# Optimization experiments

Measured on AMD Instinct MI355X. Metric: run time of the kernel, lower is better.

Reference implementation:

```python
import jax, jax.numpy as jnp
import numpy as np

LAMBDA_ENERGY = 0.1
LAMBDA_COV = 0.005
TWO_PI = 2.0 * np.pi
EPS = 1e-12


def setup_inputs() -> dict:
    key = jax.random.key(0)
    k1, k2, k3, k4 = jax.random.split(key, 4)
    B, T, C, D, K, F = 32, 1024, 8, 8, 8, 64
    x = jax.random.normal(k1, (B, T, C, F), dtype=jnp.float32)
    x_hat = jax.random.normal(k2, (B, T, C, F), dtype=jnp.float32)
    z = jax.random.normal(k3, (B, T, C, D), dtype=jnp.float32)
    # gamma is a mixture-responsibility tensor (softmax output in DAGMM)
    gamma = jax.nn.softmax(jax.random.uniform(k4, (B, T, C, K), dtype=jnp.float32) * 4.0, axis=-1)
    return {"x": x, "x_hat": x_hat, "z": z, "gamma": gamma}


def _gmm_energy(z, gamma):
    # z: [B,T,C,D], gamma: [B,T,C,K]
    N = gamma.shape[0] * gamma.shape[1] * gamma.shape[2]
    gsum = jnp.sum(gamma, axis=(0, 1, 2))                      # [K]
    phi = gsum / N                                             # [K]
    mu = jnp.einsum('btck,btcd->kd', gamma, z) / gsum[:, None]  # [K,D]
    z_mu = z[..., None, :] - mu                                # [B,T,C,K,D]
    cov = jnp.einsum('btck,btcki,btckj->kij', gamma, z_mu, z_mu) / gsum[:, None, None]  # [K,D,D]

    D = cov.shape[-1]
    cov_k = cov + EPS * jnp.eye(D, dtype=cov.dtype)            # [K,D,D]
    cov_inv = jnp.linalg.inv(cov_k)                            # batched small-matrix inverse
    L = jnp.linalg.cholesky(TWO_PI * cov_k)                    # [K,D,D]
    det_cov = jnp.prod(jnp.diagonal(L, axis1=-2, axis2=-1), axis=-1)  # [K], = sqrt(det(2*pi*cov))
    cov_diag = jnp.sum(1.0 / jnp.diagonal(cov_k, axis1=-2, axis2=-1))

    # quadratic form per sample/component: [B,T,C,K]
    quad = jnp.einsum('btcki,kij,btckj->btck', z_mu, cov_inv, z_mu)
    E = jnp.exp(-0.5 * quad)
    E_z = -jnp.log(jnp.sum(phi * E / jnp.sqrt(det_cov), axis=-1) + EPS)
    return jnp.mean(E_z), cov_diag


def reference(x, x_hat, z, gamma):
    reconst_loss = jnp.mean((x_hat - x) ** 2)
    sample_energy, cov_diag = _gmm_energy(z, gamma)
    return reconst_loss + LAMBDA_ENERGY * sample_energy + LAMBDA_COV * cov_diag
```

## Files before the change

kernel.cpp:

```cpp
#include <hip/hip_runtime.h>
#include <math.h>

#define WS_RED   0
#define WS_EN    2048
#define WS_MU    2304
#define WS_CINV  2368
#define WS_COEF  2880
#define WS_CD    2888
#define WS_STATP 4096

static constexpr int NSAMP = 32 * 1024 * 8;
static constexpr int NX4   = NSAMP * 64 / 4;
static constexpr int RE_BLOCKS   = 2048;
static constexpr int STAT_BLOCKS = 256;
static constexpr int EN_BLOCKS   = 256;
static constexpr float EPSF = 1e-12f;

__device__ inline float wave_reduce_sum(float v) {
    #pragma unroll
    for (int m = 1; m < 64; m <<= 1) v += __shfl_xor(v, m, 64);
    return v;
}
__device__ inline double wave_reduce_sum_d(double v) {
    #pragma unroll
    for (int m = 1; m < 64; m <<= 1) v += __shfl_xor(v, m, 64);
    return v;
}

__global__ __launch_bounds__(256) void krecon(const float4* __restrict__ x,
                                              const float4* __restrict__ xh,
                                              float* __restrict__ ws) {
    __shared__ float lds[4];
    float acc = 0.f;
    const int t = blockIdx.x * 256 + threadIdx.x;
    #pragma unroll 4
    for (int i = 0; i < 8; ++i) {
        int idx = t + i * (RE_BLOCKS * 256);
        float4 a = x[idx], b = xh[idx];
        float d0 = b.x - a.x, d1 = b.y - a.y, d2 = b.z - a.z, d3 = b.w - a.w;
        acc = fmaf(d0, d0, acc);
        acc = fmaf(d1, d1, acc);
        acc = fmaf(d2, d2, acc);
        acc = fmaf(d3, d3, acc);
    }
    acc = wave_reduce_sum(acc);
    int w = threadIdx.x >> 6;
    if ((threadIdx.x & 63) == 0) lds[w] = acc;
    __syncthreads();
    if (threadIdx.x == 0)
        ws[WS_RED + blockIdx.x] = lds[0] + lds[1] + lds[2] + lds[3];
}

__global__ __launch_bounds__(256) void kstats(const float4* __restrict__ z4,
                                              const float* __restrict__ gamma,
                                              float* __restrict__ ws) {
    __shared__ float lds[4][360];
    float acc[45];
    #pragma unroll
    for (int i = 0; i < 45; ++i) acc[i] = 0.f;

    const int k    = threadIdx.x & 7;
    const int grp  = (blockIdx.x << 5) | (threadIdx.x >> 3);
    constexpr int NGRP  = STAT_BLOCKS << 5;
    constexpr int ITERS = NSAMP / NGRP;

    for (int it = 0; it < ITERS; ++it) {
        int n = grp + it * NGRP;
        float4 a = z4[n * 2], b = z4[n * 2 + 1];
        float zv[8] = {a.x, a.y, a.z, a.w, b.x, b.y, b.z, b.w};
        float g = gamma[n * 8 + k];
        acc[0] += g;
        float gz[8];
        #pragma unroll
        for (int i = 0; i < 8; ++i) { gz[i] = g * zv[i]; acc[1 + i] += gz[i]; }
        #pragma unroll
        for (int i = 0; i < 8; ++i) {
            #pragma unroll
            for (int j = 0; j < 8; ++j) {
                if (j <= i)
                    acc[9 + (i * (i + 1)) / 2 + j] =
                        fmaf(gz[i], zv[j], acc[9 + (i * (i + 1)) / 2 + j]);
            }
        }
    }

    #pragma unroll
    for (int i = 0; i < 45; ++i) {
        float v = acc[i];
        v += __shfl_xor(v, 8, 64);
        v += __shfl_xor(v, 16, 64);
        v += __shfl_xor(v, 32, 64);
        acc[i] = v;
    }
    int lane = threadIdx.x & 63, w = threadIdx.x >> 6;
    if (lane < 8) {
        #pragma unroll
        for (int i = 0; i < 45; ++i) lds[w][lane * 45 + i] = acc[i];
    }
    __syncthreads();
    for (int v = threadIdx.x; v < 360; v += 256) {
        ws[WS_STATP + blockIdx.x * 360 + v] =
            lds[0][v] + lds[1][v] + lds[2][v] + lds[3][v];
    }
}

__global__ void kfinalize(float* __restrict__ ws) {
    __shared__ double sstat[360];
    for (int v = threadIdx.x; v < 360; v += 512) {
        double s = 0.0;
        for (int b = 0; b < STAT_BLOCKS; ++b)
            s += (double)ws[WS_STATP + b * 360 + v];
        sstat[v] = s;
    }
    __syncthreads();

    int k = threadIdx.x;
    if (k < 8) {
        const double* st = &sstat[k * 45];
        double g = st[0];
        double mu[8];
        for (int d = 0; d < 8; ++d) mu[d] = st[1 + d] / g;
        double A[8][8];
        {
            int t = 0;
            for (int i = 0; i < 8; ++i)
                for (int j = 0; j <= i; ++j) {
                    double v = st[9 + t] / g - mu[i] * mu[j];
                    A[i][j] = v; A[j][i] = v; ++t;
                }
        }
        for (int d = 0; d < 8; ++d) A[d][d] += (double)EPSF;

        double cd = 0.0;
        for (int d = 0; d < 8; ++d) cd += 1.0 / A[d][d];
        ws[WS_CD + k] = (float)cd;

        double L[8][8] = {};
        for (int i = 0; i < 8; ++i) {
            for (int j = 0; j <= i; ++j) {
                double s = A[i][j];
                for (int p = 0; p < j; ++p) s -= L[i][p] * L[j][p];
                if (i == j) L[i][i] = sqrt(s);
                else        L[i][j] = s / L[j][j];
            }
        }
        double M[8][8] = {};
        for (int i = 0; i < 8; ++i) {
            M[i][i] = 1.0 / L[i][i];
            for (int j = 0; j < i; ++j) {
                double s = 0.0;
                for (int p = j; p < i; ++p) s -= L[i][p] * M[p][j];
                M[i][j] = s / L[i][i];
            }
        }
        for (int i = 0; i < 8; ++i)
            for (int j = 0; j < 8; ++j) {
                double s = 0.0;
                int p0 = i > j ? i : j;
                for (int p = p0; p < 8; ++p) s += M[p][i] * M[p][j];
                ws[WS_CINV + k * 64 + i * 8 + j] = (float)s;
            }

        double det = 1.0;
        for (int d = 0; d < 8; ++d) det *= L[d][d];
        double c = 2.0 * M_PI;
        det *= c * c * c * c;
        double phi = g / (double)NSAMP;
        ws[WS_COEF + k] = (float)(phi / sqrt(det));
        for (int d = 0; d < 8; ++d) ws[WS_MU + k * 8 + d] = (float)mu[d];
    }
}

__global__ __launch_bounds__(256, 4) void kenergy(const float4* __restrict__ z4,
                                                  float* __restrict__ ws) {
    __shared__ float smu[64], scinv[512], scoef[8];
    __shared__ float lds[4];
    for (int i = threadIdx.x; i < 64; i += 256) smu[i] = ws[WS_MU + i];
    for (int i = threadIdx.x; i < 512; i += 256) scinv[i] = ws[WS_CINV + i];
    if (threadIdx.x < 8) scoef[threadIdx.x] = ws[WS_COEF + threadIdx.x];
    __syncthreads();

    const int base = blockIdx.x * 1024 + threadIdx.x;
    float zv[4][8];
    #pragma unroll
    for (int s = 0; s < 4; ++s) {
        int n = base + s * 256;
        float4 a = z4[n * 2], b = z4[n * 2 + 1];
        zv[s][0] = a.x; zv[s][1] = a.y; zv[s][2] = a.z; zv[s][3] = a.w;
        zv[s][4] = b.x; zv[s][5] = b.y; zv[s][6] = b.z; zv[s][7] = b.w;
    }
    float sacc[4] = {0.f, 0.f, 0.f, 0.f};

    #pragma unroll 1
    for (int k = 0; k < 8; ++k) {
        float muk[8];
        #pragma unroll
        for (int i = 0; i < 8; ++i) muk[i] = smu[k * 8 + i];
        float dv[4][8];
        float quad[4];
        #pragma unroll
        for (int s = 0; s < 4; ++s) {
            quad[s] = 0.f;
            #pragma unroll
            for (int i = 0; i < 8; ++i) dv[s][i] = zv[s][i] - muk[i];
        }
        #pragma unroll
        for (int i = 0; i < 8; ++i) {
            float4 c0 = *(const float4*)&scinv[k * 64 + i * 8];
            float4 c1 = *(const float4*)&scinv[k * 64 + i * 8 + 4];
            #pragma unroll
            for (int s = 0; s < 4; ++s) {
                float r;
                r = c0.x * dv[s][0];
                r = fmaf(c0.y, dv[s][1], r);
                r = fmaf(c0.z, dv[s][2], r);
                r = fmaf(c0.w, dv[s][3], r);
                r = fmaf(c1.x, dv[s][4], r);
                r = fmaf(c1.y, dv[s][5], r);
                r = fmaf(c1.z, dv[s][6], r);
                r = fmaf(c1.w, dv[s][7], r);
                quad[s] = fmaf(dv[s][i], r, quad[s]);
            }
        }
        float coef = scoef[k];
        #pragma unroll
        for (int s = 0; s < 4; ++s)
            sacc[s] = fmaf(coef, __expf(-0.5f * quad[s]), sacc[s]);
    }

    float acc = 0.f;
    #pragma unroll
    for (int s = 0; s < 4; ++s) acc += -__logf(sacc[s] + EPSF);

    acc = wave_reduce_sum(acc);
    int w = threadIdx.x >> 6;
    if ((threadIdx.x & 63) == 0) lds[w] = acc;
    __syncthreads();
    if (threadIdx.x == 0)
        ws[WS_EN + blockIdx.x] = lds[0] + lds[1] + lds[2] + lds[3];
}

__global__ void kfinal(const float* __restrict__ ws, float* __restrict__ out) {
    __shared__ double ldsR[4], ldsE[4];
    double accR = 0.0, accE = 0.0;
    for (int i = threadIdx.x; i < RE_BLOCKS; i += 256) accR += (double)ws[WS_RED + i];
    for (int i = threadIdx.x; i < EN_BLOCKS; i += 256) accE += (double)ws[WS_EN + i];
    accR = wave_reduce_sum_d(accR);
    accE = wave_reduce_sum_d(accE);
    int w = threadIdx.x >> 6;
    if ((threadIdx.x & 63) == 0) { ldsR[w] = accR; ldsE[w] = accE; }
    __syncthreads();
    if (threadIdx.x == 0) {
        double R = ldsR[0] + ldsR[1] + ldsR[2] + ldsR[3];
        double E = ldsE[0] + ldsE[1] + ldsE[2] + ldsE[3];
        double cd = 0.0;
        for (int k = 0; k < 8; ++k) cd += (double)ws[WS_CD + k];
        double loss = R / ((double)NSAMP * 64.0)
                    + 0.1 * (E / (double)NSAMP)
                    + 0.005 * cd;
        out[0] = (float)loss;
    }
}

extern "C" void kernel_launch(void* const* d_in, const int* in_sizes, int n_in,
                              void* d_out, int out_size, void* d_ws, size_t ws_size,
                              hipStream_t stream) {
    const float* x     = (const float*)d_in[0];
    const float* xh    = (const float*)d_in[1];
    const float* z     = (const float*)d_in[2];
    const float* gamma = (const float*)d_in[3];
    float* ws = (float*)d_ws;

    krecon<<<RE_BLOCKS, 256, 0, stream>>>((const float4*)x, (const float4*)xh, ws);
    kstats<<<STAT_BLOCKS, 256, 0, stream>>>((const float4*)z, gamma, ws);
    kfinalize<<<1, 512, 0, stream>>>(ws);
    kenergy<<<EN_BLOCKS, 256, 0, stream>>>((const float4*)z, ws);
    kfinal<<<1, 256, 0, stream>>>(ws, (float*)d_out);
}
```

Measured before the change: 203.0 us.

## Batch loads in reduction kernels and spread energy kernel across more blocks

The reconstruction kernel now issues all eight x and x_hat float4 loads before any arithmetic and sums into four independent accumulators. The stats kernel batches loads for four iterations at a time. The energy kernel processes one sample per thread over 1024 blocks instead of four samples per thread over 256, and the workspace offsets move so the larger per-block energy array fits. The finalize and final kernels unroll their partial-sum loops with split accumulators. The goal is more memory-level parallelism and occupancy, at the cost of more registers per thread and less reuse of the covariance loads per sample in the energy kernel.

Result: no change. 199.8 us (-1.6%).

```diff
diff --git a/kernel.cpp b/kernel.cpp
--- a/kernel.cpp
+++ b/kernel.cpp
@@ -3,17 +3,17 @@
 
 #define WS_RED   0
 #define WS_EN    2048
-#define WS_MU    2304
-#define WS_CINV  2368
-#define WS_COEF  2880
-#define WS_CD    2888
+#define WS_MU    3072
+#define WS_CINV  3136
+#define WS_COEF  3648
+#define WS_CD    3656
 #define WS_STATP 4096
 
 static constexpr int NSAMP = 32 * 1024 * 8;
 static constexpr int NX4   = NSAMP * 64 / 4;
 static constexpr int RE_BLOCKS   = 2048;
 static constexpr int STAT_BLOCKS = 256;
-static constexpr int EN_BLOCKS   = 256;
+static constexpr int EN_BLOCKS   = 1024;
 static constexpr float EPSF = 1e-12f;
 
 __device__ inline float wave_reduce_sum(float v) {
@@ -31,18 +31,28 @@
                                               const float4* __restrict__ xh,
                                               float* __restrict__ ws) {
     __shared__ float lds[4];
-    float acc = 0.f;
     const int t = blockIdx.x * 256 + threadIdx.x;
-    #pragma unroll 4
+
+    float4 xa[8], xb[8];
+    #pragma unroll
+    for (int i = 0; i < 8; ++i) xa[i] = x[t + i * (RE_BLOCKS * 256)];
+    #pragma unroll
+    for (int i = 0; i < 8; ++i) xb[i] = xh[t + i * (RE_BLOCKS * 256)];
+
+    float a0 = 0.f, a1 = 0.f, a2 = 0.f, a3 = 0.f;
+    #pragma unroll
     for (int i = 0; i < 8; ++i) {
-        int idx = t + i * (RE_BLOCKS * 256);
-        float4 a = x[idx], b = xh[idx];
-        float d0 = b.x - a.x, d1 = b.y - a.y, d2 = b.z - a.z, d3 = b.w - a.w;
-        acc = fmaf(d0, d0, acc);
-        acc = fmaf(d1, d1, acc);
-        acc = fmaf(d2, d2, acc);
-        acc = fmaf(d3, d3, acc);
-    }
+        float d0 = xb[i].x - xa[i].x;
+        float d1 = xb[i].y - xa[i].y;
+        float d2 = xb[i].z - xa[i].z;
+        float d3 = xb[i].w - xa[i].w;
+        a0 = fmaf(d0, d0, a0);
+        a1 = fmaf(d1, d1, a1);
+        a2 = fmaf(d2, d2, a2);
+        a3 = fmaf(d3, d3, a3);
+    }
+    float acc = (a0 + a1) + (a2 + a3);
+
     acc = wave_reduce_sum(acc);
     int w = threadIdx.x >> 6;
     if ((threadIdx.x & 63) == 0) lds[w] = acc;
@@ -64,22 +74,33 @@
     constexpr int NGRP  = STAT_BLOCKS << 5;
     constexpr int ITERS = NSAMP / NGRP;
 
-    for (int it = 0; it < ITERS; ++it) {
-        int n = grp + it * NGRP;
-        float4 a = z4[n * 2], b = z4[n * 2 + 1];
-        float zv[8] = {a.x, a.y, a.z, a.w, b.x, b.y, b.z, b.w};
-        float g = gamma[n * 8 + k];
-        acc[0] += g;
-        float gz[8];
-        #pragma unroll
-        for (int i = 0; i < 8; ++i) { gz[i] = g * zv[i]; acc[1 + i] += gz[i]; }
-        #pragma unroll
-        for (int i = 0; i < 8; ++i) {
+    for (int it = 0; it < ITERS; it += 4) {
+        float4 za[4], zb[4];
+        float gg[4];
+        #pragma unroll
+        for (int u = 0; u < 4; ++u) {
+            int n = grp + (it + u) * NGRP;
+            za[u] = z4[n * 2];
+            zb[u] = z4[n * 2 + 1];
+            gg[u] = gamma[n * 8 + k];
+        }
+        #pragma unroll
+        for (int u = 0; u < 4; ++u) {
+            float zv[8] = {za[u].x, za[u].y, za[u].z, za[u].w,
+                           zb[u].x, zb[u].y, zb[u].z, zb[u].w};
+            float g = gg[u];
+            acc[0] += g;
+            float gz[8];
             #pragma unroll
-            for (int j = 0; j < 8; ++j) {
-                if (j <= i)
-                    acc[9 + (i * (i + 1)) / 2 + j] =
-                        fmaf(gz[i], zv[j], acc[9 + (i * (i + 1)) / 2 + j]);
+            for (int i = 0; i < 8; ++i) { gz[i] = g * zv[i]; acc[1 + i] += gz[i]; }
+            #pragma unroll
+            for (int i = 0; i < 8; ++i) {
+                #pragma unroll
+                for (int j = 0; j < 8; ++j) {
+                    if (j <= i)
+                        acc[9 + (i * (i + 1)) / 2 + j] =
+                            fmaf(gz[i], zv[j], acc[9 + (i * (i + 1)) / 2 + j]);
+                }
             }
         }
     }
@@ -106,11 +127,18 @@
 
 __global__ void kfinalize(float* __restrict__ ws) {
     __shared__ double sstat[360];
-    for (int v = threadIdx.x; v < 360; v += 512) {
-        double s = 0.0;
-        for (int b = 0; b < STAT_BLOCKS; ++b)
-            s += (double)ws[WS_STATP + b * 360 + v];
-        sstat[v] = s;
+    int v = threadIdx.x;
+    if (v < 360) {
+        const float* p = &ws[WS_STATP + v];
+        double s0 = 0.0, s1 = 0.0, s2 = 0.0, s3 = 0.0;
+        #pragma unroll 4
+        for (int b = 0; b < STAT_BLOCKS; b += 4) {
+            s0 += (double)p[(b + 0) * 360];
+            s1 += (double)p[(b + 1) * 360];
+            s2 += (double)p[(b + 2) * 360];
+            s3 += (double)p[(b + 3) * 360];
+        }
+        sstat[v] = (s0 + s1) + (s2 + s3);
     }
     __syncthreads();
 
@@ -125,8 +153,8 @@
             int t = 0;
             for (int i = 0; i < 8; ++i)
                 for (int j = 0; j <= i; ++j) {
-                    double v = st[9 + t] / g - mu[i] * mu[j];
-                    A[i][j] = v; A[j][i] = v; ++t;
+                    double val = st[9 + t] / g - mu[i] * mu[j];
+                    A[i][j] = val; A[j][i] = val; ++t;
                 }
         }
         for (int d = 0; d < 8; ++d) A[d][d] += (double)EPSF;
@@ -180,57 +208,36 @@
     if (threadIdx.x < 8) scoef[threadIdx.x] = ws[WS_COEF + threadIdx.x];
     __syncthreads();
 
-    const int base = blockIdx.x * 1024 + threadIdx.x;
-    float zv[4][8];
-    #pragma unroll
-    for (int s = 0; s < 4; ++s) {
-        int n = base + s * 256;
-        float4 a = z4[n * 2], b = z4[n * 2 + 1];
-        zv[s][0] = a.x; zv[s][1] = a.y; zv[s][2] = a.z; zv[s][3] = a.w;
-        zv[s][4] = b.x; zv[s][5] = b.y; zv[s][6] = b.z; zv[s][7] = b.w;
-    }
-    float sacc[4] = {0.f, 0.f, 0.f, 0.f};
+    const int n = blockIdx.x * 256 + threadIdx.x;
+    float4 a = z4[n * 2], b = z4[n * 2 + 1];
+    float zv[8] = {a.x, a.y, a.z, a.w, b.x, b.y, b.z, b.w};
+    float sacc = 0.f;
 
     #pragma unroll 1
     for (int k = 0; k < 8; ++k) {
-        float muk[8];
-        #pragma unroll
-        for (int i = 0; i < 8; ++i) muk[i] = smu[k * 8 + i];
-        float dv[4][8];
-        float quad[4];
-        #pragma unroll
-        for (int s = 0; s < 4; ++s) {
-            quad[s] = 0.f;
-            #pragma unroll
-            for (int i = 0; i < 8; ++i) dv[s][i] = zv[s][i] - muk[i];
-        }
+        float dv[8];
+        #pragma unroll
+        for (int i = 0; i < 8; ++i) dv[i] = zv[i] - smu[k * 8 + i];
+        float quad = 0.f;
         #pragma unroll
         for (int i = 0; i < 8; ++i) {
             float4 c0 = *(const float4*)&scinv[k * 64 + i * 8];
             float4 c1 = *(const float4*)&scinv[k * 64 + i * 8 + 4];
-            #pragma unroll
-            for (int s = 0; s < 4; ++s) {
-                float r;
-                r = c0.x * dv[s][0];
-                r = fmaf(c0.y, dv[s][1], r);
-                r = fmaf(c0.z, dv[s][2], r);
-                r = fmaf(c0.w, dv[s][3], r);
-                r = fmaf(c1.x, dv[s][4], r);
-                r = fmaf(c1.y, dv[s][5], r);
-                r = fmaf(c1.z, dv[s][6], r);
-                r = fmaf(c1.w, dv[s][7], r);
-                quad[s] = fmaf(dv[s][i], r, quad[s]);
-            }
-        }
-        float coef = scoef[k];
-        #pragma unroll
-        for (int s = 0; s < 4; ++s)
-            sacc[s] = fmaf(coef, __expf(-0.5f * quad[s]), sacc[s]);
-    }
-
-    float acc = 0.f;
-    #pragma unroll
-    for (int s = 0; s < 4; ++s) acc += -__logf(sacc[s] + EPSF);
+            float r;
+            r = c0.x * dv[0];
+            r = fmaf(c0.y, dv[1], r);
+            r = fmaf(c0.z, dv[2], r);
+            r = fmaf(c0.w, dv[3], r);
+            r = fmaf(c1.x, dv[4], r);
+            r = fmaf(c1.y, dv[5], r);
+            r = fmaf(c1.z, dv[6], r);
+            r = fmaf(c1.w, dv[7], r);
+            quad = fmaf(dv[i], r, quad);
+        }
+        sacc = fmaf(scoef[k], __expf(-0.5f * quad), sacc);
+    }
+
+    float acc = -__logf(sacc + EPSF);
 
     acc = wave_reduce_sum(acc);
     int w = threadIdx.x >> 6;
@@ -243,7 +250,9 @@
 __global__ void kfinal(const float* __restrict__ ws, float* __restrict__ out) {
     __shared__ double ldsR[4], ldsE[4];
     double accR = 0.0, accE = 0.0;
+    #pragma unroll 4
     for (int i = threadIdx.x; i < RE_BLOCKS; i += 256) accR += (double)ws[WS_RED + i];
+    #pragma unroll 4
     for (int i = threadIdx.x; i < EN_BLOCKS; i += 256) accE += (double)ws[WS_EN + i];
     accR = wave_reduce_sum_d(accR);
     accE = wave_reduce_sum_d(accE);
```
